# Kernel tuning notes

Measured on AMD Instinct MI355X. Metric: run time of the kernel, lower is better.

Reference implementation:

```python
import jax, jax.numpy as jnp
import numpy as np

EMBED_DIM = 1024
NUM_HEADS = 16
HEAD_DIM = EMBED_DIM // NUM_HEADS
B, SQ, SK = 4, 2048, 2048


def setup_inputs() -> dict:
    key = jax.random.key(0)
    ks = jax.random.split(key, 8)
    d = EMBED_DIM
    # xavier-uniform-like scale for projection weights
    lim = float(np.sqrt(6.0 / (d + d)))
    def w(k):
        return jax.random.uniform(k, (d, d), jnp.float32, -lim, lim)
    return {
        "q": jax.random.normal(ks[0], (B, SQ, d), jnp.float32),
        "k": jax.random.normal(ks[1], (B, SK, d), jnp.float32),
        "v": jax.random.normal(ks[2], (B, SK, d), jnp.float32),
        "Wq": w(ks[3]), "bq": jnp.zeros((d,), jnp.float32),
        "Wk": w(ks[4]), "bk": jnp.zeros((d,), jnp.float32),
        "Wv": w(ks[5]), "bv": jnp.zeros((d,), jnp.float32),
        "Wo": w(ks[6]), "bo": jnp.zeros((d,), jnp.float32),
    }


def reference(q, k, v, Wq, bq, Wk, bk, Wv, bv, Wo, bo):
    # nn.Linear applies x @ W.T + b
    Bq = q.shape[0]
    scale = HEAD_DIM ** (-0.5)
    def split_heads(x):  # [B, S, D] -> [B, H, S, Hd]
        return x.reshape(Bq, -1, NUM_HEADS, HEAD_DIM).transpose(0, 2, 1, 3)
    _q = split_heads(q @ Wq.T + bq)
    _k = split_heads(k @ Wk.T + bk)
    _v = split_heads(v @ Wv.T + bv)
    attn = jnp.einsum("bhqd,bhkd->bhqk", _q, _k) * scale
    attn = jax.nn.softmax(attn, axis=-1)
    x = jnp.einsum("bhqk,bhkd->bhqd", attn, _v)
    x = x.transpose(0, 2, 1, 3).reshape(Bq, -1, EMBED_DIM)
    x = x @ Wo.T + bo
    return (x, attn)
```

## Files before the change

kernel.cpp:

```cpp
#include <hip/hip_runtime.h>
#include <hip/hip_bf16.h>


typedef _Float16 h4 __attribute__((ext_vector_type(4)));
typedef _Float16 h8 __attribute__((ext_vector_type(8)));
typedef float f4 __attribute__((ext_vector_type(4)));

#define EMBED 1024
#define HEADS 16
#define HD 64
#define BB 4
#define SS 2048
#define MROWS (BB * SS)

#define GLD(src, dst)                                                                  \
  __builtin_amdgcn_global_load_lds((const __attribute__((address_space(1))) void*)(src), \
                                   (__attribute__((address_space(3))) void*)(dst), 16, 0, 0)

__device__ inline float fexp2(float x) {
  float r;
  asm("v_exp_f32 %0, %1" : "=v"(r) : "v"(x));
  return r;
}

__global__ __launch_bounds__(256) void cast3_f32_f16(const float* __restrict__ a,
                                                     const float* __restrict__ b,
                                                     const float* __restrict__ c,
                                                     _Float16* __restrict__ oa,
                                                     _Float16* __restrict__ ob,
                                                     _Float16* __restrict__ oc, int n) {
  const float* in = blockIdx.y == 0 ? a : blockIdx.y == 1 ? b : c;
  _Float16* out = blockIdx.y == 0 ? oa : blockIdx.y == 1 ? ob : oc;
  int i = (blockIdx.x * 256 + threadIdx.x) * 4;
  if (i < n) {
    float4 v = *reinterpret_cast<const float4*>(in + i);
    h4 o = {(_Float16)v.x, (_Float16)v.y, (_Float16)v.z, (_Float16)v.w};
    *reinterpret_cast<h4*>(out + i) = o;
  }
}

__global__ __launch_bounds__(256) void cast4_f32_f16(const float* __restrict__ a,
                                                     const float* __restrict__ b,
                                                     const float* __restrict__ c,
                                                     const float* __restrict__ d,
                                                     _Float16* __restrict__ oa,
                                                     _Float16* __restrict__ ob,
                                                     _Float16* __restrict__ oc,
                                                     _Float16* __restrict__ od, int n) {
  const float* in = blockIdx.y == 0 ? a : blockIdx.y == 1 ? b : blockIdx.y == 2 ? c : d;
  _Float16* out = blockIdx.y == 0 ? oa : blockIdx.y == 1 ? ob : blockIdx.y == 2 ? oc : od;
  int i = (blockIdx.x * 256 + threadIdx.x) * 4;
  if (i < n) {
    float4 v = *reinterpret_cast<const float4*>(in + i);
    h4 o = {(_Float16)v.x, (_Float16)v.y, (_Float16)v.z, (_Float16)v.w};
    *reinterpret_cast<h4*>(out + i) = o;
  }
}

template <int OUTF32>
__device__ __forceinline__ void gemm_body(const _Float16* __restrict__ A,
                                          const _Float16* __restrict__ W,
                                          const float* __restrict__ bias,
                                          void* __restrict__ out, char* smem) {
  char* la = smem;
  char* lb = smem + 16384;
  const int t = threadIdx.x;
  const int lane = t & 63;
  const int w = t >> 6;
  const int g = lane >> 4, r16 = lane & 15;
  const int wr = (w >> 1) * 64, wc = (w & 1) * 64;
  const int m0 = blockIdx.x * 128, n0 = blockIdx.y * 128;
  const int p_in_wave = (w << 10) + (lane << 4);

  const char* Ab = (const char*)A;
  const char* Wb = (const char*)W;

  f4 acc[4][4] = {};

  for (int kt = 0; kt < EMBED; kt += 64) {
#pragma unroll
    for (int c = 0; c < 4; c++) {
      int p0 = c * 4096 + p_in_wave;
      int row = p0 >> 7;
      int scol = (p0 & 127) ^ ((row & 7) << 4);
      GLD(Ab + ((size_t)(m0 + row) * EMBED + kt) * 2 + scol, la + c * 4096 + (w << 10));
      GLD(Wb + ((size_t)(n0 + row) * EMBED + kt) * 2 + scol, lb + c * 4096 + (w << 10));
    }
    __syncthreads();
    const int sw = (r16 & 7) << 4;
#pragma unroll
    for (int kk = 0; kk < 2; kk++) {
      h8 af[4], bf[4];
#pragma unroll
      for (int m = 0; m < 4; m++)
        af[m] = *(const h8*)(la + (wr + m * 16 + r16) * 128 + ((kk * 64 + 16 * g) ^ sw));
#pragma unroll
      for (int n = 0; n < 4; n++)
        bf[n] = *(const h8*)(lb + (wc + n * 16 + r16) * 128 + ((kk * 64 + 16 * g) ^ sw));
#pragma unroll
      for (int m = 0; m < 4; m++)
#pragma unroll
        for (int n = 0; n < 4; n++)
          acc[m][n] = __builtin_amdgcn_mfma_f32_16x16x32_f16(af[m], bf[n], acc[m][n], 0, 0, 0);
    }
    __syncthreads();
  }

#pragma unroll
  for (int n = 0; n < 4; n++) {
    int gc = n0 + wc + n * 16 + r16;
    float bv = bias[gc];
#pragma unroll
    for (int m = 0; m < 4; m++) {
#pragma unroll
      for (int r = 0; r < 4; r++) {
        int gr = m0 + wr + m * 16 + 4 * g + r;
        float vv = acc[m][n][r] + bv;
        if (OUTF32)
          reinterpret_cast<float*>(out)[(size_t)gr * EMBED + gc] = vv;
        else
          reinterpret_cast<_Float16*>(out)[(size_t)gr * EMBED + gc] = (_Float16)vv;
      }
    }
  }
}

__global__ __launch_bounds__(256, 2) void gemm_qkv(const _Float16* qh, const _Float16* kh,
                                                   const _Float16* vh, const _Float16* wq,
                                                   const _Float16* wk, const _Float16* wv,
                                                   const float* bq, const float* bk,
                                                   const float* bv, _Float16* Q, _Float16* K,
                                                   _Float16* V) {
  __shared__ char smem[32768];
  const int z = blockIdx.z;
  const _Float16* A = z == 0 ? qh : z == 1 ? kh : vh;
  const _Float16* W = z == 0 ? wq : z == 1 ? wk : wv;
  const float* bias = z == 0 ? bq : z == 1 ? bk : bv;
  _Float16* out = z == 0 ? Q : z == 1 ? K : V;
  gemm_body<0>(A, W, bias, (void*)out, smem);
}

__global__ __launch_bounds__(256, 2) void gemm_out(const _Float16* __restrict__ A,
                                                   const _Float16* __restrict__ W,
                                                   const float* __restrict__ bias,
                                                   float* __restrict__ out) {
  __shared__ char smem[32768];
  gemm_body<1>(A, W, bias, (void*)out, smem);
}

__global__ __launch_bounds__(256) void transpose_v(const _Float16* __restrict__ Vp,
                                                   _Float16* __restrict__ Vt) {
  __shared__ _Float16 tile[64][72];
  const int s0 = blockIdx.x * 64;
  const int bh = blockIdx.y;
  const int b = bh >> 4, h = bh & 15;
  const int t = threadIdx.x;
#pragma unroll
  for (int it = 0; it < 2; it++) {
    int c = t + it * 256;
    int r = c >> 3, c8 = (c & 7) * 8;
    *reinterpret_cast<float4*>(&tile[r][c8]) =
        *reinterpret_cast<const float4*>(Vp + ((size_t)b * SS + s0 + r) * EMBED + h * HD + c8);
  }
  __syncthreads();
#pragma unroll
  for (int it = 0; it < 2; it++) {
    int c = t + it * 256;
    int d = c >> 3, s8 = (c & 7) * 8;
    int s32 = s8 & 31;
    int hf = s32 >> 4;
    int g0 = (s32 & 8) ? 2 : 0;
    h4 lo = {tile[s8 + 0][d], tile[s8 + 1][d], tile[s8 + 2][d], tile[s8 + 3][d]};
    h4 hi = {tile[s8 + 4][d], tile[s8 + 5][d], tile[s8 + 6][d], tile[s8 + 7][d]};
    _Float16* base = Vt + ((size_t)bh * HD + d) * SS + s0 + (s8 & ~31);
    *reinterpret_cast<h4*>(base + g0 * 8 + hf * 4) = lo;
    *reinterpret_cast<h4*>(base + (g0 + 1) * 8 + hf * 4) = hi;
  }
}

__global__ __launch_bounds__(256, 2) void attn_fused(const _Float16* __restrict__ Q,
                                                     const _Float16* __restrict__ K,
                                                     const _Float16* __restrict__ Vt,
                                                     float* __restrict__ attn_out,
                                                     _Float16* __restrict__ Oh) {
  __shared__ char smem[32768];
  const int t = threadIdx.x;
  const int lane = t & 63;
  const int w = t >> 6;
  const int g = lane >> 4, r16 = lane & 15;
  const int qt0 = blockIdx.x;
  const int bh = blockIdx.y;
  const int b = bh >> 4, h = bh & 15;
  const int q0 = qt0 * 64;
  const int p_in_wave = (w << 10) + (lane << 4);
  const int sw = (r16 & 7) << 4;

  const float CC = 0.1803368801f;

  const char* kbase = (const char*)K + ((size_t)b * SS * EMBED + h * HD) * 2;
  const char* vtbase = (const char*)Vt + (size_t)bh * HD * SS * 2;

  int srow[2], scol[2];
#pragma unroll
  for (int c = 0; c < 2; c++) {
    int p0 = c * 4096 + p_in_wave;
    srow[c] = p0 >> 7;
    scol[c] = (p0 & 127) ^ ((srow[c] & 7) << 4);
  }

#define STAGE_K(boff, kb)                                                              \
  {                                                                                    \
    _Pragma("unroll") for (int c = 0; c < 2; c++)                                      \
        GLD(kbase + (size_t)((kb) * 64 + srow[c]) * 2048 + scol[c],                    \
            smem + (boff) + c * 4096 + (w << 10));                                     \
  }
#define STAGE_V(boff, kb)                                                              \
  {                                                                                    \
    _Pragma("unroll") for (int c = 0; c < 2; c++)                                      \
        GLD(vtbase + (size_t)srow[c] * 4096 + (kb) * 128 + scol[c],                    \
            smem + (boff) + c * 4096 + (w << 10));                                     \
  }

  h8 qf[4][2];
#pragma unroll
  for (int qt = 0; qt < 4; qt++) {
    const _Float16* qptr = Q + ((size_t)b * SS + q0 + qt * 16 + r16) * EMBED + h * HD;
#pragma unroll
    for (int kk = 0; kk < 2; kk++)
      qf[qt][kk] = *reinterpret_cast<const h8*>(qptr + kk * 32 + 8 * g);
  }

  const int krowoff = (w * 16 + r16) * 128;

  float s4[4] = {0.f, 0.f, 0.f, 0.f};
  STAGE_K(0, 0);
  __syncthreads();
  for (int kb = 0; kb < 32; kb++) {
    const char* cur = smem + (kb & 1) * 8192;
    if (kb < 31) STAGE_K(((kb + 1) & 1) * 8192, kb + 1);
    h8 af0 = *(const h8*)(cur + krowoff + ((16 * g) ^ sw));
    h8 af1 = *(const h8*)(cur + krowoff + ((64 + 16 * g) ^ sw));
    __builtin_amdgcn_s_setprio(1);
#pragma unroll
    for (int qt = 0; qt < 4; qt++) {
      f4 sf = {0.f, 0.f, 0.f, 0.f};
      sf = __builtin_amdgcn_mfma_f32_16x16x32_f16(af0, qf[qt][0], sf, 0, 0, 0);
      sf = __builtin_amdgcn_mfma_f32_16x16x32_f16(af1, qf[qt][1], sf, 0, 0, 0);
      __builtin_amdgcn_s_setprio(0);
#pragma unroll
      for (int r = 0; r < 4; r++) s4[qt] += fexp2(sf[r] * CC);
      __builtin_amdgcn_s_setprio(1);
    }
    __builtin_amdgcn_s_setprio(0);
    __syncthreads();
  }
#pragma unroll
  for (int qt = 0; qt < 4; qt++) {
    s4[qt] += __shfl_xor(s4[qt], 16, 64);
    s4[qt] += __shfl_xor(s4[qt], 32, 64);
  }
  float* lds_l = (float*)smem;
  if (lane < 16) {
#pragma unroll
    for (int qt = 0; qt < 4; qt++) lds_l[w * 64 + qt * 16 + lane] = s4[qt];
  }
  __syncthreads();
  float lgr[4];
#pragma unroll
  for (int qt = 0; qt < 4; qt++) {
    int qi = qt * 16 + r16;
    lgr[qt] = -__log2f(lds_l[qi] + lds_l[64 + qi] + lds_l[128 + qi] + lds_l[192 + qi]);
  }
  __syncthreads();

  f4 oacc[4][4] = {};
  const int voff = ((w >> 1) * 64 + g * 16 + (w & 1) * 8) ^ sw;

  STAGE_K(0, 0);
  STAGE_V(16384, 0);
  __syncthreads();
  for (int kb = 0; kb < 32; kb++) {
    const char* ck = smem + (kb & 1) * 8192;
    const char* cv = smem + 16384 + (kb & 1) * 8192;
    if (kb < 31) {
      STAGE_K(((kb + 1) & 1) * 8192, kb + 1);
      STAGE_V(16384 + ((kb + 1) & 1) * 8192, kb + 1);
    }
    h8 af0 = *(const h8*)(ck + krowoff + ((16 * g) ^ sw));
    h8 af1 = *(const h8*)(ck + krowoff + ((64 + 16 * g) ^ sw));
    h4 pa[4];
    __builtin_amdgcn_s_setprio(1);
#pragma unroll
    for (int qt = 0; qt < 4; qt++) {
      f4 sf = {0.f, 0.f, 0.f, 0.f};
      sf = __builtin_amdgcn_mfma_f32_16x16x32_f16(af0, qf[qt][0], sf, 0, 0, 0);
      sf = __builtin_amdgcn_mfma_f32_16x16x32_f16(af1, qf[qt][1], sf, 0, 0, 0);
      __builtin_amdgcn_s_setprio(0);
      float a0 = fexp2(fmaf(sf[0], CC, lgr[qt]));
      float a1 = fexp2(fmaf(sf[1], CC, lgr[qt]));
      float a2 = fexp2(fmaf(sf[2], CC, lgr[qt]));
      float a3 = fexp2(fmaf(sf[3], CC, lgr[qt]));
      f4 st = {a0, a1, a2, a3};
      __builtin_nontemporal_store(
          st, reinterpret_cast<f4*>(attn_out + ((size_t)bh * SS + q0 + qt * 16 + r16) * SS +
                                    kb * 64 + w * 16 + 4 * g));
      pa[qt] = h4{(_Float16)a0, (_Float16)a1, (_Float16)a2, (_Float16)a3};
      __builtin_amdgcn_s_setprio(1);
    }
#pragma unroll
    for (int dt = 0; dt < 4; dt++) {
      h4 vf = *(const h4*)(cv + (dt * 16 + r16) * 128 + voff);
#pragma unroll
      for (int qt = 0; qt < 4; qt++)
        oacc[qt][dt] = __builtin_amdgcn_mfma_f32_16x16x16f16(pa[qt], vf, oacc[qt][dt], 0, 0, 0);
    }
    __builtin_amdgcn_s_setprio(0);
    __syncthreads();
  }

  float* ro = (float*)(smem + (w & 1) * 16384);
  if (w < 2) {
#pragma unroll
    for (int qt = 0; qt < 4; qt++)
#pragma unroll
      for (int dt = 0; dt < 4; dt++)
#pragma unroll
        for (int r = 0; r < 4; r++)
          ro[(qt * 16 + 4 * g + r) * 64 + dt * 16 + r16] = oacc[qt][dt][r];
  }
  __syncthreads();
  if (w >= 2) {
#pragma unroll
    for (int qt = 0; qt < 4; qt++)
#pragma unroll
      for (int dt = 0; dt < 4; dt++)
#pragma unroll
        for (int r = 0; r < 4; r++) {
          int a = (qt * 16 + 4 * g + r) * 64 + dt * 16 + r16;
          ro[a] += oacc[qt][dt][r];
        }
  }
  __syncthreads();
  {
    const float* r0 = (const float*)smem;
    const float* r1 = (const float*)(smem + 16384);
    int q = t >> 2, d0 = (t & 3) * 16;
    _Float16* orow = Oh + ((size_t)b * SS + q0 + q) * EMBED + h * HD + d0;
    h8 o0, o1;
#pragma unroll
    for (int i = 0; i < 8; i++)
      o0[i] = (_Float16)(r0[q * 64 + d0 + i] + r1[q * 64 + d0 + i]);
#pragma unroll
    for (int i = 0; i < 8; i++)
      o1[i] = (_Float16)(r0[q * 64 + d0 + 8 + i] + r1[q * 64 + d0 + 8 + i]);
    *reinterpret_cast<h8*>(orow) = o0;
    *reinterpret_cast<h8*>(orow + 8) = o1;
  }
#undef STAGE_K
#undef STAGE_V
}

extern "C" void kernel_launch(void* const* d_in, const int* in_sizes, int n_in,
                              void* d_out, int out_size, void* d_ws, size_t ws_size,
                              hipStream_t stream) {
  const float* q  = (const float*)d_in[0];
  const float* k  = (const float*)d_in[1];
  const float* v  = (const float*)d_in[2];
  const float* Wq = (const float*)d_in[3];
  const float* bq = (const float*)d_in[4];
  const float* Wk = (const float*)d_in[5];
  const float* bk = (const float*)d_in[6];
  const float* Wv = (const float*)d_in[7];
  const float* bv = (const float*)d_in[8];
  const float* Wo = (const float*)d_in[9];
  const float* bo = (const float*)d_in[10];

  const size_t NW = (size_t)EMBED * EMBED;
  const size_t NX = (size_t)MROWS * EMBED;

  if (ws_size < (4 * NW + 6 * NX) * sizeof(_Float16)) return;
  _Float16* ws  = (_Float16*)d_ws;
  _Float16* wqh = ws;
  _Float16* wkh = wqh + NW;
  _Float16* wvh = wkh + NW;
  _Float16* woh = wvh + NW;
  _Float16* qh  = woh + NW;
  _Float16* kh  = qh + NX;
  _Float16* vh  = kh + NX;
  _Float16* Qh  = vh + NX;
  _Float16* Kh  = Qh + NX;
  _Float16* Vph = Kh + NX;
  _Float16* Vt2 = qh;
  _Float16* OhA = kh;

  float* xout = (float*)d_out;
  float* attn = xout + NX;

  cast3_f32_f16<<<dim3((NX / 4 + 255) / 256, 3), dim3(256), 0, stream>>>(q, k, v, qh, kh, vh,
                                                                         (int)NX);
  cast4_f32_f16<<<dim3((NW / 4 + 255) / 256, 4), dim3(256), 0, stream>>>(
      Wq, Wk, Wv, Wo, wqh, wkh, wvh, woh, (int)NW);

  dim3 ggrid(MROWS / 128, EMBED / 128), gblk(256);
  gemm_qkv<<<dim3(MROWS / 128, EMBED / 128, 3), gblk, 0, stream>>>(qh, kh, vh, wqh, wkh, wvh,
                                                                   bq, bk, bv, Qh, Kh, Vph);

  transpose_v<<<dim3(SS / 64, BB * HEADS), dim3(256), 0, stream>>>(Vph, Vt2);

  attn_fused<<<dim3(SS / 64, BB * HEADS), dim3(256), 0, stream>>>(Qh, Kh, Vt2, attn, OhA);

  gemm_out<<<ggrid, gblk, 0, stream>>>(OhA, woh, bo, xout);
}
```

Measured before the change: 465.1 us.

## Give each wave private K/V LDS staging and replace block barriers with vmcnt waits

```diff
diff --git a/kernel.cpp b/kernel.cpp
--- a/kernel.cpp
+++ b/kernel.cpp
@@ -16,6 +16,12 @@
 #define GLD(src, dst)                                                                  \
   __builtin_amdgcn_global_load_lds((const __attribute__((address_space(1))) void*)(src), \
                                    (__attribute__((address_space(3))) void*)(dst), 16, 0, 0)
+
+#define WAITV(N)                                                                       \
+  {                                                                                    \
+    asm volatile("s_waitcnt vmcnt(" #N ")" ::: "memory");                              \
+    __builtin_amdgcn_sched_barrier(0);                                                 \
+  }
 
 __device__ inline float fexp2(float x) {
   float r;
@@ -167,14 +173,11 @@
   for (int it = 0; it < 2; it++) {
     int c = t + it * 256;
     int d = c >> 3, s8 = (c & 7) * 8;
-    int s32 = s8 & 31;
-    int hf = s32 >> 4;
-    int g0 = (s32 & 8) ? 2 : 0;
     h4 lo = {tile[s8 + 0][d], tile[s8 + 1][d], tile[s8 + 2][d], tile[s8 + 3][d]};
     h4 hi = {tile[s8 + 4][d], tile[s8 + 5][d], tile[s8 + 6][d], tile[s8 + 7][d]};
-    _Float16* base = Vt + ((size_t)bh * HD + d) * SS + s0 + (s8 & ~31);
-    *reinterpret_cast<h4*>(base + g0 * 8 + hf * 4) = lo;
-    *reinterpret_cast<h4*>(base + (g0 + 1) * 8 + hf * 4) = hi;
+    _Float16* dst = Vt + ((size_t)bh * HD + d) * SS + s0 + s8;
+    *reinterpret_cast<h4*>(dst) = lo;
+    *reinterpret_cast<h4*>(dst + 4) = hi;
   }
 }
 
@@ -183,7 +186,7 @@
                                                      const _Float16* __restrict__ Vt,
                                                      float* __restrict__ attn_out,
                                                      _Float16* __restrict__ Oh) {
-  __shared__ char smem[32768];
+  __shared__ char smem[33792];
   const int t = threadIdx.x;
   const int lane = t & 63;
   const int w = t >> 6;
@@ -192,7 +195,6 @@
   const int bh = blockIdx.y;
   const int b = bh >> 4, h = bh & 15;
   const int q0 = qt0 * 64;
-  const int p_in_wave = (w << 10) + (lane << 4);
   const int sw = (r16 & 7) << 4;
 
   const float CC = 0.1803368801f;
@@ -200,25 +202,28 @@
   const char* kbase = (const char*)K + ((size_t)b * SS * EMBED + h * HD) * 2;
   const char* vtbase = (const char*)Vt + (size_t)bh * HD * SS * 2;
 
-  int srow[2], scol[2];
-#pragma unroll
-  for (int c = 0; c < 2; c++) {
-    int p0 = c * 4096 + p_in_wave;
-    srow[c] = p0 >> 7;
-    scol[c] = (p0 & 127) ^ ((srow[c] & 7) << 4);
-  }
-
-#define STAGE_K(boff, kb)                                                              \
+  const int kst_row = lane >> 3;
+  const int kst_piece = lane & 7;
+
+  char* const kreg = smem + w * 4096;
+  char* const vreg = smem + 16384 + w * 4096;
+
+#define STAGE_KW(buf, kb)                                                              \
   {                                                                                    \
-    _Pragma("unroll") for (int c = 0; c < 2; c++)                                      \
-        GLD(kbase + (size_t)((kb) * 64 + srow[c]) * 2048 + scol[c],                    \
-            smem + (boff) + c * 4096 + (w << 10));                                     \
-  }
-#define STAGE_V(boff, kb)                                                              \
+    _Pragma("unroll") for (int c = 0; c < 2; c++) {                                    \
+      int row = c * 8 + kst_row;                                                       \
+      int sp = (kst_piece * 16) ^ ((row & 7) << 4);                                    \
+      GLD(kbase + (size_t)((kb) * 64 + w * 16 + row) * 2048 + sp,                      \
+          kreg + (buf) * 2048 + (c * 64 + lane) * 16);                                 \
+    }                                                                                  \
+  }
+#define STAGE_VW(buf, kb)                                                              \
   {                                                                                    \
-    _Pragma("unroll") for (int c = 0; c < 2; c++)                                      \
-        GLD(vtbase + (size_t)srow[c] * 4096 + (kb) * 128 + scol[c],                    \
-            smem + (boff) + c * 4096 + (w << 10));                                     \
+    _Pragma("unroll") for (int c = 0; c < 2; c++) {                                    \
+      int flat = c * 64 + lane;                                                        \
+      GLD(vtbase + (size_t)(flat >> 1) * 4096 + (kb) * 128 + w * 32 + (flat & 1) * 16, \
+          vreg + (buf) * 2048 + flat * 16);                                            \
+    }                                                                                  \
   }
 
   h8 qf[4][2];
@@ -230,16 +235,19 @@
       qf[qt][kk] = *reinterpret_cast<const h8*>(qptr + kk * 32 + 8 * g);
   }
 
-  const int krowoff = (w * 16 + r16) * 128;
-
   float s4[4] = {0.f, 0.f, 0.f, 0.f};
-  STAGE_K(0, 0);
-  __syncthreads();
+  STAGE_KW(0, 0);
   for (int kb = 0; kb < 32; kb++) {
-    const char* cur = smem + (kb & 1) * 8192;
-    if (kb < 31) STAGE_K(((kb + 1) & 1) * 8192, kb + 1);
-    h8 af0 = *(const h8*)(cur + krowoff + ((16 * g) ^ sw));
-    h8 af1 = *(const h8*)(cur + krowoff + ((64 + 16 * g) ^ sw));
+    const int buf = kb & 1;
+    if (kb < 31) {
+      STAGE_KW(buf ^ 1, kb + 1);
+      WAITV(2);
+    } else {
+      WAITV(0);
+    }
+    const char* kp = kreg + buf * 2048 + r16 * 128;
+    h8 af0 = *(const h8*)(kp + ((16 * g) ^ sw));
+    h8 af1 = *(const h8*)(kp + ((64 + 16 * g) ^ sw));
     __builtin_amdgcn_s_setprio(1);
 #pragma unroll
     for (int qt = 0; qt < 4; qt++) {
@@ -252,14 +260,13 @@
       __builtin_amdgcn_s_setprio(1);
     }
     __builtin_amdgcn_s_setprio(0);
-    __syncthreads();
   }
 #pragma unroll
   for (int qt = 0; qt < 4; qt++) {
     s4[qt] += __shfl_xor(s4[qt], 16, 64);
     s4[qt] += __shfl_xor(s4[qt], 32, 64);
   }
-  float* lds_l = (float*)smem;
+  float* lds_l = (float*)(smem + 32768);
   if (lane < 16) {
 #pragma unroll
     for (int qt = 0; qt < 4; qt++) lds_l[w * 64 + qt * 16 + lane] = s4[qt];
@@ -271,23 +278,27 @@
     int qi = qt * 16 + r16;
     lgr[qt] = -__log2f(lds_l[qi] + lds_l[64 + qi] + lds_l[128 + qi] + lds_l[192 + qi]);
   }
-  __syncthreads();
 
   f4 oacc[4][4] = {};
-  const int voff = ((w >> 1) * 64 + g * 16 + (w & 1) * 8) ^ sw;
-
-  STAGE_K(0, 0);
-  STAGE_V(16384, 0);
-  __syncthreads();
+
+  STAGE_KW(0, 0);
+  STAGE_VW(0, 0);
   for (int kb = 0; kb < 32; kb++) {
-    const char* ck = smem + (kb & 1) * 8192;
-    const char* cv = smem + 16384 + (kb & 1) * 8192;
-    if (kb < 31) {
-      STAGE_K(((kb + 1) & 1) * 8192, kb + 1);
-      STAGE_V(16384 + ((kb + 1) & 1) * 8192, kb + 1);
-    }
-    h8 af0 = *(const h8*)(ck + krowoff + ((16 * g) ^ sw));
-    h8 af1 = *(const h8*)(ck + krowoff + ((64 + 16 * g) ^ sw));
+    const int buf = kb & 1;
+    if (kb == 0) {
+      STAGE_KW(1, 1);
+      STAGE_VW(1, 1);
+      WAITV(4);
+    } else if (kb < 31) {
+      STAGE_KW(buf ^ 1, kb + 1);
+      STAGE_VW(buf ^ 1, kb + 1);
+      WAITV(8);
+    } else {
+      WAITV(4);
+    }
+    const char* kp = kreg + buf * 2048 + r16 * 128;
+    h8 af0 = *(const h8*)(kp + ((16 * g) ^ sw));
+    h8 af1 = *(const h8*)(kp + ((64 + 16 * g) ^ sw));
     h4 pa[4];
     __builtin_amdgcn_s_setprio(1);
 #pragma unroll
@@ -307,17 +318,18 @@
       pa[qt] = h4{(_Float16)a0, (_Float16)a1, (_Float16)a2, (_Float16)a3};
       __builtin_amdgcn_s_setprio(1);
     }
+    const char* vp = vreg + buf * 2048;
 #pragma unroll
     for (int dt = 0; dt < 4; dt++) {
-      h4 vf = *(const h4*)(cv + (dt * 16 + r16) * 128 + voff);
+      h4 vf = *(const h4*)(vp + (dt * 16 + r16) * 32 + 8 * g);
 #pragma unroll
       for (int qt = 0; qt < 4; qt++)
         oacc[qt][dt] = __builtin_amdgcn_mfma_f32_16x16x16f16(pa[qt], vf, oacc[qt][dt], 0, 0, 0);
     }
     __builtin_amdgcn_s_setprio(0);
-    __syncthreads();
-  }
-
+  }
+
+  __syncthreads();
   float* ro = (float*)(smem + (w & 1) * 16384);
   if (w < 2) {
 #pragma unroll
@@ -356,8 +368,8 @@
     *reinterpret_cast<h8*>(orow) = o0;
     *reinterpret_cast<h8*>(orow + 8) = o1;
   }
-#undef STAGE_K
-#undef STAGE_V
+#undef STAGE_KW
+#undef STAGE_VW
 }
 
 extern "C" void kernel_launch(void* const* d_in, const int* in_sizes, int n_in,
```

New measurement: 444.4 us. 4.5% less time.
